# Performance work log

Hardware: AMD Instinct MI355X
Metric: run time of the kernel (lower is better)

## Reference

```python
import math
import jax, jax.numpy as jnp
import numpy as np

B, L, H, E = 2, 2048, 8, 64
S, D = 2048, 64


def _row_mask(index, sub_len, win_len, log_l):
    # Faithful to torch code, including the swapped-arg call convention:
    # called with sub_len = L (query len), win_len = S (key len).
    mask = np.zeros(win_len, dtype=np.float32)
    if (win_len // sub_len) * 2 * log_l > index:
        mask[: index + 1] = 1.0
    else:
        while index >= 0:
            if index - log_l + 1 < 0:
                mask[:index] = 1.0
                break
            mask[index - log_l + 1 : index + 1] = 1.0
            for i in range(log_l):
                new_index = index - log_l + 1 - 2 ** i
                if index - new_index <= sub_len and new_index >= 0:
                    mask[new_index] = 1.0
            index -= sub_len
    return mask


def _log_mask(win_len, sub_len):
    # mirrors LogSparseAttention.log_mask(L, S) with its swapped row_mask call
    log_l = math.ceil(np.log2(win_len))  # log2 of query length L
    m = np.zeros((win_len, sub_len), dtype=np.float32)
    for i in range(win_len):
        m[i] = _row_mask(i, win_len, sub_len, log_l)
    return jnp.asarray(m)[None, None]  # [1,1,L,S]


_MASK = _log_mask(L, S)


def setup_inputs() -> dict:
    key = jax.random.key(0)
    kq, kk, kv = jax.random.split(key, 3)
    return {
        "queries": jax.random.normal(kq, (B, L, H, E), dtype=jnp.float32),
        "keys": jax.random.normal(kk, (B, S, H, E), dtype=jnp.float32),
        "values": jax.random.normal(kv, (B, S, H, D), dtype=jnp.float32),
        "attention_mask": jnp.ones((1,), dtype=bool),  # unused, as in the torch module
    }


def reference(queries, keys, values, attention_mask):
    scale = 1.0 / math.sqrt(queries.shape[-1])
    scores = jnp.einsum("blhe,bshe->bhls", queries, keys)  # [B,H,L,S]
    mask = _MASK[:, :, : scores.shape[-2], : scores.shape[-1]]
    scores = scores * mask + (-1e9) * (1.0 - mask)
    A = jax.nn.softmax(scale * scores, axis=-1)  # dropout = identity in eval
    V = jnp.einsum("bhls,bshd->blhd", A, values)  # [B,L,H,D]
    return V
```

## Files before the change

kernel.cpp:

```cpp
#include <hip/hip_runtime.h>


#define BB 2
#define LL 2048
#define HH 8
#define EE 64
#define SS 2048

__global__ __launch_bounds__(256) void logsparse_attn_kernel(
    const float* __restrict__ Q,
    const float* __restrict__ K,
    const float* __restrict__ V,
    float* __restrict__ O)
{
    const int lane = threadIdx.x & 63;
    const int wv   = threadIdx.x >> 6;
    const int row  = blockIdx.x * 4 + wv;
    const int l  = row % LL;
    const int bh = row / LL;
    const int h  = bh % HH;
    const int b  = bh / HH;

    const int t = lane & 15;
    const int g = lane >> 4;

    const float scale = 0.125f;

    const size_t qbase = (((size_t)b * LL + l) * HH + h) * (size_t)EE;
    const float4 qf = *(const float4*)(Q + qbase + 4 * t);

    const float* Kb = K + ((size_t)b * SS * HH + (size_t)h) * 0 + ((size_t)b * SS * HH * EE + (size_t)h * EE);
    const float* Vb = V + ((size_t)b * SS * HH * EE + (size_t)h * EE);

    int ntaps, nkeys, w0;
    if (l < 22) { ntaps = 0; nkeys = l + 1; w0 = 0; }
    else {
        w0 = l - 10;
        ntaps = 32 - __clz(w0);
        if (ntaps > 11) ntaps = 11;
        nkeys = ntaps + 11;
    }
    const int nchunks = (nkeys + 3) >> 2;

    float  m  = -1e30f;
    float  lw = 0.0f;
    float4 acc = {0.f, 0.f, 0.f, 0.f};

    for (int c = 0; c < nchunks; ++c) {
        const int n      = 4 * c + g;
        const bool valid = (n < nkeys);
        const int nc     = valid ? n : (nkeys - 1);
        int key;
        if (l < 22)           key = nc;
        else if (nc < ntaps)  key = w0 - (1 << (ntaps - 1 - nc));
        else                  key = w0 + (nc - ntaps);
        const size_t off = ((size_t)key << 9) + 4 * t;
        const float4 kf = *(const float4*)(Kb + off);
        const float4 vf = *(const float4*)(Vb + off);

        float p = qf.x * kf.x + qf.y * kf.y + qf.z * kf.z + qf.w * kf.w;
        p += __shfl_xor(p, 1, 64);
        p += __shfl_xor(p, 2, 64);
        p += __shfl_xor(p, 4, 64);
        p += __shfl_xor(p, 8, 64);
        const float score = valid ? p * scale : -1e30f;

        float cm = score;
        cm = fmaxf(cm, __shfl_xor(cm, 16, 64));
        cm = fmaxf(cm, __shfl_xor(cm, 32, 64));
        const float mn    = fmaxf(m, cm);
        const float alpha = __expf(m - mn);
        const float wj    = __expf(score - mn);
        lw    = lw    * alpha + wj;
        acc.x = acc.x * alpha + wj * vf.x;
        acc.y = acc.y * alpha + wj * vf.y;
        acc.z = acc.z * alpha + wj * vf.z;
        acc.w = acc.w * alpha + wj * vf.w;
        m = mn;
    }

    lw    += __shfl_xor(lw, 16, 64);    lw    += __shfl_xor(lw, 32, 64);
    acc.x += __shfl_xor(acc.x, 16, 64); acc.x += __shfl_xor(acc.x, 32, 64);
    acc.y += __shfl_xor(acc.y, 16, 64); acc.y += __shfl_xor(acc.y, 32, 64);
    acc.z += __shfl_xor(acc.z, 16, 64); acc.z += __shfl_xor(acc.z, 32, 64);
    acc.w += __shfl_xor(acc.w, 16, 64); acc.w += __shfl_xor(acc.w, 32, 64);

    if (g == 0) {
        const float inv = 1.0f / lw;
        float4 o;
        o.x = acc.x * inv; o.y = acc.y * inv; o.z = acc.z * inv; o.w = acc.w * inv;
        *(float4*)(O + qbase + 4 * t) = o;
    }
}

extern "C" void kernel_launch(void* const* d_in, const int* in_sizes, int n_in,
                              void* d_out, int out_size, void* d_ws, size_t ws_size,
                              hipStream_t stream) {
    const float* Q = (const float*)d_in[0];
    const float* K = (const float*)d_in[1];
    const float* V = (const float*)d_in[2];
    float* O = (float*)d_out;

    const int rows   = BB * HH * LL;
    const int blocks = rows / 4;
    hipLaunchKernelGGL(logsparse_attn_kernel, dim3(blocks), dim3(256), 0, stream,
                       Q, K, V, O);
}
```

Measured before the change: 94.06 us.

## Fully unroll key loop, batch loads, and use DPP reductions for dot products

Replaces the sequential online-softmax loop with a fixed 6-chunk unrolled loop that issues all K/V loads up front, computes scores, then does one max and one exp-weighted accumulation pass per lane group. The intra-16-lane dot-product reduction uses DPP row moves instead of ds_bpermute shuffles, and the cross-group max/sum merge is done once at the end. This aims to expose memory-level parallelism and cut shuffle latency, at the cost of more registers and always doing 6 chunks, including redundant clamped loads for short rows.

```diff
diff --git a/kernel.cpp b/kernel.cpp
--- a/kernel.cpp
+++ b/kernel.cpp
@@ -6,6 +6,12 @@
 #define HH 8
 #define EE 64
 #define SS 2048
+
+template<int CTRL>
+__device__ __forceinline__ float dpp_add(float v) {
+    int t = __builtin_amdgcn_mov_dpp(__float_as_int(v), CTRL, 0xF, 0xF, false);
+    return v + __int_as_float(t);
+}
 
 __global__ __launch_bounds__(256) void logsparse_attn_kernel(
     const float* __restrict__ Q,
@@ -18,19 +24,18 @@
     const int row  = blockIdx.x * 4 + wv;
     const int l  = row % LL;
     const int bh = row / LL;
-    const int h  = bh % HH;
+    const int h  = bh & (HH - 1);
     const int b  = bh / HH;
 
     const int t = lane & 15;
     const int g = lane >> 4;
 
-    const float scale = 0.125f;
-
     const size_t qbase = (((size_t)b * LL + l) * HH + h) * (size_t)EE;
     const float4 qf = *(const float4*)(Q + qbase + 4 * t);
 
-    const float* Kb = K + ((size_t)b * SS * HH + (size_t)h) * 0 + ((size_t)b * SS * HH * EE + (size_t)h * EE);
-    const float* Vb = V + ((size_t)b * SS * HH * EE + (size_t)h * EE);
+    const size_t bhoff = (size_t)b * ((size_t)SS * HH * EE) + (size_t)h * EE;
+    const float* Kb = K + bhoff;
+    const float* Vb = V + bhoff;
 
     int ntaps, nkeys, w0;
     if (l < 22) { ntaps = 0; nkeys = l + 1; w0 = 0; }
@@ -40,55 +45,63 @@
         if (ntaps > 11) ntaps = 11;
         nkeys = ntaps + 11;
     }
-    const int nchunks = (nkeys + 3) >> 2;
 
-    float  m  = -1e30f;
-    float  lw = 0.0f;
-    float4 acc = {0.f, 0.f, 0.f, 0.f};
-
-    for (int c = 0; c < nchunks; ++c) {
-        const int n      = 4 * c + g;
-        const bool valid = (n < nkeys);
-        const int nc     = valid ? n : (nkeys - 1);
+    float  sc[6];
+    float4 vv[6];
+    #pragma unroll
+    for (int c = 0; c < 6; ++c) {
+        const int n  = 4 * c + g;
+        const int nc = (n < nkeys) ? n : (nkeys - 1);
         int key;
         if (l < 22)           key = nc;
         else if (nc < ntaps)  key = w0 - (1 << (ntaps - 1 - nc));
         else                  key = w0 + (nc - ntaps);
         const size_t off = ((size_t)key << 9) + 4 * t;
         const float4 kf = *(const float4*)(Kb + off);
-        const float4 vf = *(const float4*)(Vb + off);
+        vv[c] = *(const float4*)(Vb + off);
 
         float p = qf.x * kf.x + qf.y * kf.y + qf.z * kf.z + qf.w * kf.w;
-        p += __shfl_xor(p, 1, 64);
-        p += __shfl_xor(p, 2, 64);
-        p += __shfl_xor(p, 4, 64);
-        p += __shfl_xor(p, 8, 64);
-        const float score = valid ? p * scale : -1e30f;
-
-        float cm = score;
-        cm = fmaxf(cm, __shfl_xor(cm, 16, 64));
-        cm = fmaxf(cm, __shfl_xor(cm, 32, 64));
-        const float mn    = fmaxf(m, cm);
-        const float alpha = __expf(m - mn);
-        const float wj    = __expf(score - mn);
-        lw    = lw    * alpha + wj;
-        acc.x = acc.x * alpha + wj * vf.x;
-        acc.y = acc.y * alpha + wj * vf.y;
-        acc.z = acc.z * alpha + wj * vf.z;
-        acc.w = acc.w * alpha + wj * vf.w;
-        m = mn;
+        p = dpp_add<0xB1>(p);
+        p = dpp_add<0x4E>(p);
+        p = dpp_add<0x124>(p);
+        p = dpp_add<0x128>(p);
+        sc[c] = (n < nkeys) ? p * 0.125f : -1e30f;
     }
 
-    lw    += __shfl_xor(lw, 16, 64);    lw    += __shfl_xor(lw, 32, 64);
-    acc.x += __shfl_xor(acc.x, 16, 64); acc.x += __shfl_xor(acc.x, 32, 64);
-    acc.y += __shfl_xor(acc.y, 16, 64); acc.y += __shfl_xor(acc.y, 32, 64);
-    acc.z += __shfl_xor(acc.z, 16, 64); acc.z += __shfl_xor(acc.z, 32, 64);
-    acc.w += __shfl_xor(acc.w, 16, 64); acc.w += __shfl_xor(acc.w, 32, 64);
+    float mg = sc[0];
+    #pragma unroll
+    for (int c = 1; c < 6; ++c) mg = fmaxf(mg, sc[c]);
+
+    float  lsum = 0.0f;
+    float4 acc  = {0.f, 0.f, 0.f, 0.f};
+    #pragma unroll
+    for (int c = 0; c < 6; ++c) {
+        const float w = __expf(sc[c] - mg);
+        lsum  += w;
+        acc.x += w * vv[c].x;
+        acc.y += w * vv[c].y;
+        acc.z += w * vv[c].z;
+        acc.w += w * vv[c].w;
+    }
+
+    float M = mg;
+    M = fmaxf(M, __shfl_xor(M, 16, 64));
+    M = fmaxf(M, __shfl_xor(M, 32, 64));
+    const float r = __expf(mg - M);
+    lsum  *= r;
+    acc.x *= r; acc.y *= r; acc.z *= r; acc.w *= r;
+
+    lsum  += __shfl_xor(lsum, 16, 64);    lsum  += __shfl_xor(lsum, 32, 64);
+    acc.x += __shfl_xor(acc.x, 16, 64);   acc.x += __shfl_xor(acc.x, 32, 64);
+    acc.y += __shfl_xor(acc.y, 16, 64);   acc.y += __shfl_xor(acc.y, 32, 64);
+    acc.z += __shfl_xor(acc.z, 16, 64);   acc.z += __shfl_xor(acc.z, 32, 64);
+    acc.w += __shfl_xor(acc.w, 16, 64);   acc.w += __shfl_xor(acc.w, 32, 64);
 
     if (g == 0) {
-        const float inv = 1.0f / lw;
+        const float inv = 1.0f / lsum;
         float4 o;
-        o.x = acc.x * inv; o.y = acc.y * inv; o.z = acc.z * inv; o.w = acc.w * inv;
+        o.x = acc.x * inv; o.y = acc.y * inv;
+        o.z = acc.z * inv; o.w = acc.w * inv;
         *(float4*)(O + qbase + 4 * t) = o;
     }
 }
```

Measured after the change: 92.51 us. No clear change (-1.7%).
